# Performance work log

Measured on AMD Instinct MI355X. Metric: run time of the kernel, lower is better.

## Reference

```python
import jax, jax.numpy as jnp
import numpy as np

N_HEAD = 16
D_MODEL = 1024
D_K = 64
D_V = 64
TEMPER = float(np.power(D_MODEL, 0.5))  # NOTE: source scales by sqrt(d_model), not sqrt(d_k)


def setup_inputs() -> dict:
    key = jax.random.key(0)
    ks = jax.random.split(key, 6)
    B, T = 4, 2048
    q = jax.random.normal(ks[0], (B, T, D_MODEL), dtype=jnp.float32)
    k = jax.random.normal(ks[1], (B, T, D_MODEL), dtype=jnp.float32)
    v = jax.random.normal(ks[2], (B, T, D_MODEL), dtype=jnp.float32)
    # xavier_normal for [out, in] = [n_head*d, d_model]; stored as [d_model, n_head*d] for x @ W
    def xavier(kk, fan_out, fan_in):
        std = float(np.sqrt(2.0 / (fan_in + fan_out)))
        return jax.random.normal(kk, (fan_in, fan_out), dtype=jnp.float32) * std
    W_Q = xavier(ks[3], N_HEAD * D_K, D_MODEL)
    W_K = xavier(ks[4], N_HEAD * D_K, D_MODEL)
    W_V = xavier(ks[5], N_HEAD * D_V, D_MODEL)
    return {"q": q, "k": k, "v": v, "W_Q": W_Q, "W_K": W_K, "W_V": W_V}


def reference(q, k, v, W_Q, W_K, W_V):
    B, Tq, _ = q.shape
    Tk = k.shape[1]
    residual = q
    # project and split heads: [B, T, H, d]
    qh = (q @ W_Q).reshape(B, Tq, N_HEAD, D_K)
    kh = (k @ W_K).reshape(B, Tk, N_HEAD, D_K)
    vh = (v @ W_V).reshape(B, Tk, N_HEAD, D_V)
    # scaled dot-product attention (dropout is identity in eval)
    attn = jnp.einsum('bqhd,bkhd->bhqk', qh, kh) / TEMPER
    attn = jax.nn.softmax(attn, axis=-1)
    out = jnp.einsum('bhqk,bkhd->bqhd', attn, vh).reshape(B, Tq, N_HEAD * D_V)
    return out + residual
```

## Files before the change

kernel.cpp:

```cpp
#include <hip/hip_runtime.h>
#include <cstdint>
#include <cstddef>

typedef __bf16 bf16x8 __attribute__((ext_vector_type(8)));
typedef float f32x4 __attribute__((ext_vector_type(4)));
typedef unsigned short u16;
typedef unsigned int u32;

static constexpr int T = 2048;
static constexpr int DM = 1024;
static constexpr float QSCALE = 0.04508422f;

#define GLOBAL_AS __attribute__((address_space(1)))
#define LDS_AS __attribute__((address_space(3)))

__device__ __forceinline__ void gld_lds16(const u16* g, u16* l) {
  __builtin_amdgcn_global_load_lds((const GLOBAL_AS u32*)g, (LDS_AS u32*)l, 16, 0, 0);
}

__device__ __forceinline__ u16 f2bf(float f) {
  u32 u = __builtin_bit_cast(u32, f);
  u += 0x7fffu + ((u >> 16) & 1u);
  return (u16)(u >> 16);
}

__device__ __forceinline__ u32 pkb(float lo, float hi) {
#if __has_builtin(__builtin_amdgcn_cvt_pk_bf16_f32)
  typedef __bf16 bf16x2 __attribute__((ext_vector_type(2)));
  bf16x2 r = __builtin_amdgcn_cvt_pk_bf16_f32(lo, hi);
  return __builtin_bit_cast(u32, r);
#else
  return __builtin_amdgcn_perm(__builtin_bit_cast(u32, hi),
                               __builtin_bit_cast(u32, lo), 0x07060302u);
#endif
}

__device__ __forceinline__ float fexp2(float x) {
#if __has_builtin(__builtin_amdgcn_exp2f)
  return __builtin_amdgcn_exp2f(x);
#else
  return __builtin_exp2f(x);
#endif
}

__global__ __launch_bounds__(256) void xcvt(
    const float* __restrict__ q, const float* __restrict__ k, const float* __restrict__ v,
    u16* __restrict__ oq, u16* __restrict__ ok, u16* __restrict__ ov) {
  const float* X = blockIdx.y == 0 ? q : blockIdx.y == 1 ? k : v;
  u16* O = blockIdx.y == 0 ? oq : blockIdx.y == 1 ? ok : ov;
  const size_t i = ((size_t)blockIdx.x * 256 + threadIdx.x) * 8;
  float4 a0 = *(const float4*)(X + i), a1 = *(const float4*)(X + i + 4);
  uint4 p;
  p.x = pkb(a0.x, a0.y); p.y = pkb(a0.z, a0.w);
  p.z = pkb(a1.x, a1.y); p.w = pkb(a1.z, a1.w);
  *(uint4*)(O + i) = p;
}

__global__ __launch_bounds__(256) void wt_kernel(
    const float* __restrict__ W0, const float* __restrict__ W1, const float* __restrict__ W2,
    u16* __restrict__ O0, u16* __restrict__ O1, u16* __restrict__ O2) {
  const float* W = blockIdx.z == 0 ? W0 : blockIdx.z == 1 ? W1 : W2;
  u16* O = blockIdx.z == 0 ? O0 : blockIdx.z == 1 ? O1 : O2;
  const float sc = blockIdx.z == 0 ? QSCALE : 1.0f;
  const int k0 = blockIdx.x * 64, n0 = blockIdx.y * 64;
  __shared__ float tile[64][68];
  const int tid = threadIdx.x;
#pragma unroll
  for (int it = 0; it < 4; ++it) {
    int chunk = tid + it * 256;
    int r = chunk >> 4, c4 = (chunk & 15) * 4;
    *(float4*)&tile[r][c4] = *(const float4*)(W + (size_t)(k0 + r) * DM + n0 + c4);
  }
  __syncthreads();
#pragma unroll
  for (int it = 0; it < 4; ++it) {
    int chunk = tid + it * 256;
    int n = chunk >> 4, k4 = (chunk & 15) * 4;
    ushort4 o;
    o.x = f2bf(tile[k4 + 0][n] * sc);
    o.y = f2bf(tile[k4 + 1][n] * sc);
    o.z = f2bf(tile[k4 + 2][n] * sc);
    o.w = f2bf(tile[k4 + 3][n] * sc);
    *(ushort4*)(O + (size_t)(n0 + n) * DM + k0 + k4) = o;
  }
}

__global__ __launch_bounds__(256, 3) void gemm_proj(
    const u16* __restrict__ Xq, const u16* __restrict__ Xk, const u16* __restrict__ Xv,
    const u16* __restrict__ Wq, const u16* __restrict__ Wk, const u16* __restrict__ Wv,
    u16* __restrict__ Oq, u16* __restrict__ Ok, u16* __restrict__ VHt) {
  const int z = blockIdx.y;
  const u16* X = z == 0 ? Xq : z == 1 ? Xk : Xv;
  const u16* Wt = z == 0 ? Wq : z == 1 ? Wk : Wv;
  const int xcd = blockIdx.x & 7, j = blockIdx.x >> 3;
  const int n0 = (j & 7) * 128;
  const int m0 = (xcd * 8 + (j >> 3)) * 128;
  __shared__ u16 Al[128][64];
  __shared__ u16 Bl[128][64];
  const int tid = threadIdx.x, w = tid >> 6, lane = tid & 63;
  const int c16 = lane & 15, quad = lane >> 4;
  const int wm = (w >> 1) * 64, wn = (w & 1) * 64;
  const int rk = lane >> 3;
  const int ck = ((lane & 7) ^ rk) * 8;
  const int swz = c16 & 7;
  f32x4 acc[4][4] = {};
  const u16* ga = X + (size_t)(m0 + w * 32 + rk) * DM + ck;
  const u16* gb = Wt + (size_t)(n0 + w * 32 + rk) * DM + ck;
  for (int kk = 0; kk < 1024; kk += 64) {
    __syncthreads();
#pragma unroll
    for (int i = 0; i < 4; ++i) {
      gld_lds16(ga + kk + (size_t)(i * 8) * DM, &Al[w * 32 + i * 8][0]);
      gld_lds16(gb + kk + (size_t)(i * 8) * DM, &Bl[w * 32 + i * 8][0]);
    }
    __syncthreads();
#pragma unroll
    for (int s = 0; s < 2; ++s) {
      bf16x8 af[4], bfr[4];
#pragma unroll
      for (int t = 0; t < 4; ++t) af[t] = *(const bf16x8*)&Al[wm + t * 16 + c16][((quad + 4 * s) ^ swz) * 8];
#pragma unroll
      for (int t = 0; t < 4; ++t) bfr[t] = *(const bf16x8*)&Bl[wn + t * 16 + c16][((quad + 4 * s) ^ swz) * 8];
#pragma unroll
      for (int mt = 0; mt < 4; ++mt)
#pragma unroll
        for (int nt = 0; nt < 4; ++nt)
          acc[mt][nt] = __builtin_amdgcn_mfma_f32_16x16x32_bf16(af[mt], bfr[nt], acc[mt][nt], 0, 0, 0);
    }
  }
  if (z < 2) {
    u16* O = z == 0 ? Oq : Ok;
#pragma unroll
    for (int mt = 0; mt < 4; ++mt)
#pragma unroll
      for (int nt = 0; nt < 4; ++nt)
#pragma unroll
        for (int r = 0; r < 4; ++r) {
          size_t row = m0 + wm + mt * 16 + quad * 4 + r;
          size_t col = n0 + wn + nt * 16 + c16;
          O[row * DM + col] = f2bf(acc[mt][nt][r]);
        }
  } else {
#pragma unroll
    for (int mt = 0; mt < 4; ++mt)
#pragma unroll
      for (int nt = 0; nt < 4; ++nt) {
        const int row0 = m0 + wm + mt * 16 + quad * 4;
        const int col = n0 + wn + nt * 16 + c16;
        const int bb = row0 >> 11, t0 = row0 & 2047;
        const int hh = col >> 6, dd = col & 63;
        ushort4 o;
        o.x = f2bf(acc[mt][nt][0]);
        o.y = f2bf(acc[mt][nt][1]);
        o.z = f2bf(acc[mt][nt][2]);
        o.w = f2bf(acc[mt][nt][3]);
        *(ushort4*)(VHt + ((size_t)((bb * 16 + hh) * 64 + dd)) * T + t0) = o;
      }
  }
}

__global__ __launch_bounds__(256, 2) void flash_kernel(
    const u16* __restrict__ QH, const u16* __restrict__ KH, const u16* __restrict__ VHt,
    const float* __restrict__ res, float* __restrict__ out) {
  const int blk = blockIdx.x;
  const int x = blk & 7, g = blk >> 3;
  const int bh = x * 8 + (g & 7);
  const int qb = g >> 3;
  const int b = bh >> 4, h = bh & 15;
  const int tid = threadIdx.x, w = tid >> 6, lane = tid & 63;
  const int c16 = lane & 15, quad = lane >> 4;
  const int swzq = c16 & 7;
  __shared__ u16 Kl[64][64];
  __shared__ u16 Vt[64][64];
  __shared__ u16 Pl[4][4][16][64];
  __shared__ float Ll[4][4][16];
  const int qbase = qb * 256 + w * 64;
  bf16x8 bq[4][2];
#pragma unroll
  for (int qi = 0; qi < 4; ++qi) {
    const u16* qp = QH + (size_t)(b * T + qbase + qi * 16 + c16) * DM + h * 64 + quad * 8;
    bq[qi][0] = *(const bf16x8*)qp;
    bq[qi][1] = *(const bf16x8*)(qp + 32);
  }
  f32x4 acc[4][4] = {};
  float rs[4] = {0.f, 0.f, 0.f, 0.f};
  const int rk = lane >> 3;
  const int ck8 = ((lane & 7) ^ rk) * 8;
  const u16* kg = KH + (size_t)(b * T) * DM + h * 64 + ck8;
  const u16* vg = VHt + ((size_t)bh * 64 + w * 16 + rk) * T + ck8;
  for (int kt = 0; kt < 32; ++kt) {
    __syncthreads();
    {
      const u16* kg0 = kg + (size_t)(kt * 64 + w * 16 + rk) * DM;
      gld_lds16(kg0, &Kl[w * 16][0]);
      gld_lds16(kg0 + (size_t)8 * DM, &Kl[w * 16 + 8][0]);
      const u16* vg0 = vg + kt * 64;
      gld_lds16(vg0, &Vt[w * 16][0]);
      gld_lds16(vg0 + (size_t)8 * T, &Vt[w * 16 + 8][0]);
    }
    __syncthreads();
    {
      bf16x8 ak[4][2];
#pragma unroll
      for (int mt = 0; mt < 4; ++mt) {
        const int r = mt * 16 + c16;
        ak[mt][0] = *(const bf16x8*)&Kl[r][(quad ^ swzq) * 8];
        ak[mt][1] = *(const bf16x8*)&Kl[r][((4 + quad) ^ swzq) * 8];
      }
#pragma unroll
      for (int qi = 0; qi < 4; ++qi) {
#pragma unroll
        for (int mt = 0; mt < 4; ++mt) {
          f32x4 st = {};
          st = __builtin_amdgcn_mfma_f32_16x16x32_bf16(ak[mt][0], bq[qi][0], st, 0, 0, 0);
          st = __builtin_amdgcn_mfma_f32_16x16x32_bf16(ak[mt][1], bq[qi][1], st, 0, 0, 0);
          const float p0 = fexp2(st[0]), p1 = fexp2(st[1]);
          const float p2 = fexp2(st[2]), p3 = fexp2(st[3]);
          rs[qi] += (p0 + p1) + (p2 + p3);
          uint2 pw;
          pw.x = pkb(p0, p1);
          pw.y = pkb(p2, p3);
          const int col = (((mt * 2 + (quad >> 1)) ^ swzq) * 8) + (quad & 1) * 4;
          *(uint2*)&Pl[w][qi][c16][col] = pw;
        }
      }
    }
    asm volatile("s_waitcnt lgkmcnt(0)" ::: "memory");
    bf16x8 ap[4][2];
#pragma unroll
    for (int qi = 0; qi < 4; ++qi) {
      ap[qi][0] = *(const bf16x8*)&Pl[w][qi][c16][(quad ^ swzq) * 8];
      ap[qi][1] = *(const bf16x8*)&Pl[w][qi][c16][((4 + quad) ^ swzq) * 8];
    }
#pragma unroll
    for (int nt = 0; nt < 4; ++nt) {
      const int r = nt * 16 + c16;
      const bf16x8 bv0 = *(const bf16x8*)&Vt[r][(quad ^ swzq) * 8];
      const bf16x8 bv1 = *(const bf16x8*)&Vt[r][((4 + quad) ^ swzq) * 8];
#pragma unroll
      for (int qi = 0; qi < 4; ++qi) {
        acc[qi][nt] = __builtin_amdgcn_mfma_f32_16x16x32_bf16(ap[qi][0], bv0, acc[qi][nt], 0, 0, 0);
        acc[qi][nt] = __builtin_amdgcn_mfma_f32_16x16x32_bf16(ap[qi][1], bv1, acc[qi][nt], 0, 0, 0);
      }
    }
  }
#pragma unroll
  for (int qi = 0; qi < 4; ++qi) {
    float t = rs[qi];
    t += __shfl_xor(t, 16, 64);
    t += __shfl_xor(t, 32, 64);
    if (quad == 0) Ll[w][qi][c16] = t;
  }
  asm volatile("s_waitcnt lgkmcnt(0)" ::: "memory");
#pragma unroll
  for (int qi = 0; qi < 4; ++qi) {
    const f32x4 lv = *(const f32x4*)&Ll[w][qi][quad * 4];
#pragma unroll
    for (int r = 0; r < 4; ++r) {
      const float inv = 1.0f / lv[r];
      const size_t rowbase = (size_t)(b * T + qbase + qi * 16 + quad * 4 + r) * DM + h * 64;
#pragma unroll
      for (int nt = 0; nt < 4; ++nt) {
        const size_t idx = rowbase + nt * 16 + c16;
        out[idx] = acc[qi][nt][r] * inv + res[idx];
      }
    }
  }
}

extern "C" void kernel_launch(void* const* d_in, const int* in_sizes, int n_in,
                              void* d_out, int out_size, void* d_ws, size_t ws_size,
                              hipStream_t stream) {
  const float* q = (const float*)d_in[0];
  const float* k = (const float*)d_in[1];
  const float* v = (const float*)d_in[2];
  const float* WQ = (const float*)d_in[3];
  const float* WK = (const float*)d_in[4];
  const float* WV = (const float*)d_in[5];
  char* ws = (char*)d_ws;
  const size_t PH = (size_t)8192 * 1024 * 2;
  const size_t WT = (size_t)1024 * 1024 * 2;
  u16* XqB = (u16*)d_out;
  u16* XkB = (u16*)d_out + (size_t)8192 * 1024;
  u16* XvB = (u16*)(ws);
  u16* WtQ = (u16*)(ws + PH);
  u16* WtK = (u16*)(ws + PH + WT);
  u16* WtV = (u16*)(ws + PH + 2 * WT);
  u16* QH  = (u16*)(ws + PH + 3 * WT);
  u16* KH  = (u16*)(ws + 2 * PH + 3 * WT);
  u16* VHt = (u16*)(ws + 3 * PH + 3 * WT);

  xcvt<<<dim3(4096, 3), 256, 0, stream>>>(q, k, v, XqB, XkB, XvB);
  wt_kernel<<<dim3(16, 16, 3), 256, 0, stream>>>(WQ, WK, WV, WtQ, WtK, WtV);
  gemm_proj<<<dim3(512, 3), 256, 0, stream>>>(XqB, XkB, XvB, WtQ, WtK, WtV, QH, KH, VHt);
  flash_kernel<<<512, 256, 0, stream>>>(QH, KH, VHt, q, (float*)d_out);
}
```

Measured before the change: 297.4 us.

## Double-buffer K/V tiles, permlane P transpose, halve queries per block

The flash kernel now double-buffers the K and V tiles in LDS, prefetching the next tile with async global-to-LDS loads while computing on the current one. The P matrix is turned into the MFMA A-operand layout in registers with v_permlane16/32_swap instead of a round trip through LDS. Each block handles 128 queries instead of 256, with twice as many blocks and a launch bound of 4 blocks per CU, to raise occupancy. The trade-off is that K/V are reloaded twice as often per head, and the vmcnt counts are hand-tuned, which is fragile.

```diff
diff --git a/kernel.cpp b/kernel.cpp
--- a/kernel.cpp
+++ b/kernel.cpp
@@ -41,6 +41,13 @@
 #else
   return __builtin_exp2f(x);
 #endif
+}
+
+__device__ __forceinline__ void pl16swap(u32& a, u32& b) {
+  asm("v_permlane16_swap_b32 %0, %1" : "+v"(a), "+v"(b));
+}
+__device__ __forceinline__ void pl32swap(u32& a, u32& b) {
+  asm("v_permlane32_swap_b32 %0, %1" : "+v"(a), "+v"(b));
 }
 
 __global__ __launch_bounds__(256) void xcvt(
@@ -159,7 +166,7 @@
   }
 }
 
-__global__ __launch_bounds__(256, 2) void flash_kernel(
+__global__ __launch_bounds__(256, 4) void flash_kernel(
     const u16* __restrict__ QH, const u16* __restrict__ KH, const u16* __restrict__ VHt,
     const float* __restrict__ res, float* __restrict__ out) {
   const int blk = blockIdx.x;
@@ -170,45 +177,57 @@
   const int tid = threadIdx.x, w = tid >> 6, lane = tid & 63;
   const int c16 = lane & 15, quad = lane >> 4;
   const int swzq = c16 & 7;
-  __shared__ u16 Kl[64][64];
-  __shared__ u16 Vt[64][64];
-  __shared__ u16 Pl[4][4][16][64];
-  __shared__ float Ll[4][4][16];
-  const int qbase = qb * 256 + w * 64;
-  bf16x8 bq[4][2];
-#pragma unroll
-  for (int qi = 0; qi < 4; ++qi) {
+  __shared__ u16 Kl[2][64][64];
+  __shared__ u16 Vt[2][64][64];
+  __shared__ float Ll[4][2][16];
+  const int qbase = qb * 128 + w * 32;
+  bf16x8 bq[2][2];
+#pragma unroll
+  for (int qi = 0; qi < 2; ++qi) {
     const u16* qp = QH + (size_t)(b * T + qbase + qi * 16 + c16) * DM + h * 64 + quad * 8;
     bq[qi][0] = *(const bf16x8*)qp;
     bq[qi][1] = *(const bf16x8*)(qp + 32);
   }
-  f32x4 acc[4][4] = {};
-  float rs[4] = {0.f, 0.f, 0.f, 0.f};
+  f32x4 acc[2][4] = {};
+  float rs[2] = {0.f, 0.f};
   const int rk = lane >> 3;
   const int ck8 = ((lane & 7) ^ rk) * 8;
   const u16* kg = KH + (size_t)(b * T) * DM + h * 64 + ck8;
   const u16* vg = VHt + ((size_t)bh * 64 + w * 16 + rk) * T + ck8;
+  {
+    const u16* kg0 = kg + (size_t)(w * 16 + rk) * DM;
+    gld_lds16(kg0, &Kl[0][w * 16][0]);
+    gld_lds16(kg0 + (size_t)8 * DM, &Kl[0][w * 16 + 8][0]);
+    gld_lds16(vg, &Vt[0][w * 16][0]);
+    gld_lds16(vg + 8 * T, &Vt[0][w * 16 + 8][0]);
+  }
+  int cur = 0;
   for (int kt = 0; kt < 32; ++kt) {
-    __syncthreads();
-    {
-      const u16* kg0 = kg + (size_t)(kt * 64 + w * 16 + rk) * DM;
-      gld_lds16(kg0, &Kl[w * 16][0]);
-      gld_lds16(kg0 + (size_t)8 * DM, &Kl[w * 16 + 8][0]);
-      const u16* vg0 = vg + kt * 64;
-      gld_lds16(vg0, &Vt[w * 16][0]);
-      gld_lds16(vg0 + (size_t)8 * T, &Vt[w * 16 + 8][0]);
-    }
-    __syncthreads();
+    __builtin_amdgcn_s_barrier();
+    if (kt < 31) {
+      const u16* kg0 = kg + (size_t)((kt + 1) * 64 + w * 16 + rk) * DM;
+      gld_lds16(kg0, &Kl[cur ^ 1][w * 16][0]);
+      gld_lds16(kg0 + (size_t)8 * DM, &Kl[cur ^ 1][w * 16 + 8][0]);
+      const u16* vg0 = vg + (kt + 1) * 64;
+      gld_lds16(vg0, &Vt[cur ^ 1][w * 16][0]);
+      gld_lds16(vg0 + (size_t)8 * T, &Vt[cur ^ 1][w * 16 + 8][0]);
+      asm volatile("s_waitcnt vmcnt(4)" ::: "memory");
+    } else {
+      asm volatile("s_waitcnt vmcnt(0)" ::: "memory");
+    }
+    __builtin_amdgcn_s_barrier();
+    bf16x8 ap[2][2];
     {
       bf16x8 ak[4][2];
 #pragma unroll
       for (int mt = 0; mt < 4; ++mt) {
         const int r = mt * 16 + c16;
-        ak[mt][0] = *(const bf16x8*)&Kl[r][(quad ^ swzq) * 8];
-        ak[mt][1] = *(const bf16x8*)&Kl[r][((4 + quad) ^ swzq) * 8];
-      }
-#pragma unroll
-      for (int qi = 0; qi < 4; ++qi) {
+        ak[mt][0] = *(const bf16x8*)&Kl[cur][r][(quad ^ swzq) * 8];
+        ak[mt][1] = *(const bf16x8*)&Kl[cur][r][((4 + quad) ^ swzq) * 8];
+      }
+#pragma unroll
+      for (int qi = 0; qi < 2; ++qi) {
+        u32 d[2][2][2];
 #pragma unroll
         for (int mt = 0; mt < 4; ++mt) {
           f32x4 st = {};
@@ -217,35 +236,38 @@
           const float p0 = fexp2(st[0]), p1 = fexp2(st[1]);
           const float p2 = fexp2(st[2]), p3 = fexp2(st[3]);
           rs[qi] += (p0 + p1) + (p2 + p3);
-          uint2 pw;
-          pw.x = pkb(p0, p1);
-          pw.y = pkb(p2, p3);
-          const int col = (((mt * 2 + (quad >> 1)) ^ swzq) * 8) + (quad & 1) * 4;
-          *(uint2*)&Pl[w][qi][c16][col] = pw;
+          d[mt >> 1][mt & 1][0] = pkb(p0, p1);
+          d[mt >> 1][mt & 1][1] = pkb(p2, p3);
         }
-      }
-    }
-    asm volatile("s_waitcnt lgkmcnt(0)" ::: "memory");
-    bf16x8 ap[4][2];
-#pragma unroll
-    for (int qi = 0; qi < 4; ++qi) {
-      ap[qi][0] = *(const bf16x8*)&Pl[w][qi][c16][(quad ^ swzq) * 8];
-      ap[qi][1] = *(const bf16x8*)&Pl[w][qi][c16][((4 + quad) ^ swzq) * 8];
+        pl32swap(d[0][0][0], d[0][1][0]);
+        pl32swap(d[0][0][1], d[0][1][1]);
+        pl32swap(d[1][0][0], d[1][1][0]);
+        pl32swap(d[1][0][1], d[1][1][1]);
+        pl16swap(d[0][0][0], d[0][1][0]);
+        pl16swap(d[0][0][1], d[0][1][1]);
+        pl16swap(d[1][0][0], d[1][1][0]);
+        pl16swap(d[1][0][1], d[1][1][1]);
+        uint4 a0 = {d[0][0][0], d[0][0][1], d[0][1][0], d[0][1][1]};
+        uint4 a1 = {d[1][0][0], d[1][0][1], d[1][1][0], d[1][1][1]};
+        ap[qi][0] = __builtin_bit_cast(bf16x8, a0);
+        ap[qi][1] = __builtin_bit_cast(bf16x8, a1);
+      }
     }
 #pragma unroll
     for (int nt = 0; nt < 4; ++nt) {
       const int r = nt * 16 + c16;
-      const bf16x8 bv0 = *(const bf16x8*)&Vt[r][(quad ^ swzq) * 8];
-      const bf16x8 bv1 = *(const bf16x8*)&Vt[r][((4 + quad) ^ swzq) * 8];
-#pragma unroll
-      for (int qi = 0; qi < 4; ++qi) {
+      const bf16x8 bv0 = *(const bf16x8*)&Vt[cur][r][(quad ^ swzq) * 8];
+      const bf16x8 bv1 = *(const bf16x8*)&Vt[cur][r][((4 + quad) ^ swzq) * 8];
+#pragma unroll
+      for (int qi = 0; qi < 2; ++qi) {
         acc[qi][nt] = __builtin_amdgcn_mfma_f32_16x16x32_bf16(ap[qi][0], bv0, acc[qi][nt], 0, 0, 0);
         acc[qi][nt] = __builtin_amdgcn_mfma_f32_16x16x32_bf16(ap[qi][1], bv1, acc[qi][nt], 0, 0, 0);
       }
     }
-  }
-#pragma unroll
-  for (int qi = 0; qi < 4; ++qi) {
+    cur ^= 1;
+  }
+#pragma unroll
+  for (int qi = 0; qi < 2; ++qi) {
     float t = rs[qi];
     t += __shfl_xor(t, 16, 64);
     t += __shfl_xor(t, 32, 64);
@@ -253,7 +275,7 @@
   }
   asm volatile("s_waitcnt lgkmcnt(0)" ::: "memory");
 #pragma unroll
-  for (int qi = 0; qi < 4; ++qi) {
+  for (int qi = 0; qi < 2; ++qi) {
     const f32x4 lv = *(const f32x4*)&Ll[w][qi][quad * 4];
 #pragma unroll
     for (int r = 0; r < 4; ++r) {
@@ -293,5 +315,5 @@
   xcvt<<<dim3(4096, 3), 256, 0, stream>>>(q, k, v, XqB, XkB, XvB);
   wt_kernel<<<dim3(16, 16, 3), 256, 0, stream>>>(WQ, WK, WV, WtQ, WtK, WtV);
   gemm_proj<<<dim3(512, 3), 256, 0, stream>>>(XqB, XkB, XvB, WtQ, WtK, WtV, QH, KH, VHt);
-  flash_kernel<<<512, 256, 0, stream>>>(QH, KH, VHt, q, (float*)d_out);
-}
+  flash_kernel<<<1024, 256, 0, stream>>>(QH, KH, VHt, q, (float*)d_out);
+}
```

Measured after the change: 279.2 us, median of 2. 1.06x faster.
